# Kernel tuning notes

Measured on AMD Instinct MI355X. Metric: run time of the kernel, lower is better.

## Reference

```python
import jax, jax.numpy as jnp
import numpy as np

BITS = 4
PACK = 32 // BITS  # 8 nibbles per int32
MASK = (1 << BITS) - 1


def _dequant_gptq(qweight, qzeros, scales):
    """GPTQ int4 dequantization matching MixedPrecisionLinear._dequantize_gptq_weight.

    qweight: [OC//PACK, IC] int32 (nibbles packed along output-channel rows)
    qzeros:  [G, IC//PACK]  int32 (nibbles packed along IC columns)
    scales:  [G, IC]        float32
    returns: [OC, IC]       float32 dequantized weight (pre-transpose)
    """
    Rp, IC = qweight.shape
    OC = Rp * PACK
    G = qzeros.shape[0]
    g = OC // G  # group size along OC

    # Unpack weights: row r*PACK + k comes from packed row r, shift k*BITS
    shifts = jnp.arange(PACK, dtype=jnp.int32) * BITS  # [PACK]
    Wq = ((qweight[:, None, :] >> shifts[None, :, None]) & MASK).reshape(OC, IC)

    # Unpack zero points per (group, ic)
    col = jnp.arange(IC, dtype=jnp.int32)
    qz_cols = qzeros[:, col // PACK]                       # [G, IC]
    zp = (qz_cols >> ((col % PACK) * BITS)[None, :]) & MASK  # [G, IC]

    zp_full = jnp.repeat(zp, g, axis=0)                    # [OC, IC]
    scales_full = jnp.repeat(scales, g, axis=0)            # [OC, IC]
    return (Wq - zp_full).astype(jnp.float32) * scales_full


def setup_inputs() -> dict:
    key = jax.random.key(0)
    k0, k1, k2, k3, k4 = jax.random.split(key, 5)
    IN, OUT, G = 4096, 11008, 32   # in_features (OC, packed), out_features (IC), groups
    N = 4096                        # flattened batch*seq tokens
    qweight = jax.random.randint(k0, (IN // PACK, OUT), 0, 2147483647, dtype=jnp.int32)
    qzeros = jax.random.randint(k1, (G, OUT // PACK), 0, 2147483647, dtype=jnp.int32)
    scales = jax.random.uniform(k2, (G, OUT), dtype=jnp.float32) * 0.01
    x = jax.random.normal(k3, (N, IN), dtype=jnp.float32)
    bias = jax.random.normal(k4, (OUT,), dtype=jnp.float32) * 0.01
    return {"input": x, "qweight": qweight, "qzeros": qzeros, "scales": scales, "bias": bias}


def reference(input, qweight, qzeros, scales, bias):
    # W_deq is [OC=in_features, IC=out_features]; the module returns W_deq.t() as the
    # linear weight, so F.linear(input, W_deq.t()) == input @ W_deq + bias.
    W = _dequant_gptq(qweight, qzeros, scales)
    return input @ W + bias
```

## Files before the change

### kernel.cpp

```cpp
#include <hip/hip_runtime.h>
#include <hip/hip_bf16.h>
#include <stdint.h>

#define M_DIM 4096
#define N_DIM 11008
#define K_DIM 4096

typedef float f32x4 __attribute__((ext_vector_type(4)));
typedef __bf16 bf16x8 __attribute__((ext_vector_type(8)));
typedef unsigned short u16x8 __attribute__((ext_vector_type(8)));
typedef unsigned short u16x4 __attribute__((ext_vector_type(4)));

typedef __attribute__((address_space(1))) const unsigned int guint;
typedef __attribute__((address_space(3))) unsigned int luint;
#define GLOAD_LDS16(g, l) \
    __builtin_amdgcn_global_load_lds((guint*)(g), (luint*)(l), 16, 0, 0)

#define WAIT_VM4() asm volatile("s_waitcnt vmcnt(4)" ::: "memory")
#define WAIT_VM0() asm volatile("s_waitcnt vmcnt(0)" ::: "memory")

__device__ __forceinline__ unsigned short f2bf(float f) {
    union { float f; unsigned u; } v; v.f = f;
    return (unsigned short)((v.u + 0x7FFFu + ((v.u >> 16) & 1u)) >> 16);
}

#define DQ_BLOCKS  ((N_DIM / 64) * (K_DIM / 256))
#define CVT_BLOCKS 2048
#define CVT_TOTAL  ((size_t)M_DIM * K_DIM)

__global__ void __launch_bounds__(256) prep_kernel(
    const float* __restrict__ X, const int* __restrict__ QW,
    const int* __restrict__ QZ, const float* __restrict__ SC,
    __hip_bfloat16* __restrict__ Xbf, __hip_bfloat16* __restrict__ Wt)
{
    const int bid = blockIdx.x;
    if (bid >= CVT_BLOCKS) {
        const int db  = bid - CVT_BLOCKS;
        const int bx  = db % (N_DIM / 64);
        const int by  = db / (N_DIM / 64);
        const int n   = bx * 64 + (threadIdx.x & 63);
        const int k64 = by * 4 + (threadIdx.x >> 6);
        const int g   = k64 >> 1;
        const int zp  = ((unsigned)QZ[g * (N_DIM / 8) + (n >> 3)]
                         >> ((n & 7) << 2)) & 15;
        const float sc = SC[g * N_DIM + n];
        const float zs = (float)zp * sc;
        unsigned qv[8];
        #pragma unroll
        for (int r = 0; r < 8; ++r)
            qv[r] = (unsigned)QW[(size_t)(k64 * 8 + r) * N_DIM + n];
        #pragma unroll
        for (int r = 0; r < 8; ++r) {
            bf16x8 h;
            #pragma unroll
            for (int j = 0; j < 8; ++j)
                h[j] = (__bf16)((float)((qv[r] >> (j * 4)) & 15u) * sc - zs);
            *reinterpret_cast<bf16x8*>(Wt + (size_t)n * K_DIM + k64 * 64 + r * 8) = h;
        }
    } else {
        const size_t nthreads = (size_t)CVT_BLOCKS * 256;
        size_t i = ((size_t)bid * 256 + threadIdx.x) * 8;
        const size_t stride = nthreads * 8;
        for (; i < CVT_TOTAL; i += stride) {
            f32x4 a = __builtin_nontemporal_load(
                reinterpret_cast<const f32x4*>(X + i));
            f32x4 b = __builtin_nontemporal_load(
                reinterpret_cast<const f32x4*>(X + i + 4));
            bf16x8 h;
            #pragma unroll
            for (int e = 0; e < 4; ++e) { h[e] = (__bf16)a[e]; h[e + 4] = (__bf16)b[e]; }
            *reinterpret_cast<bf16x8*>(Xbf + i) = h;
        }
    }
}

__global__ void __launch_bounds__(512, 2) gemm_bf16_kernel(
    const __hip_bfloat16* __restrict__ A,
    const __hip_bfloat16* __restrict__ Bt,
    const float* __restrict__ BIAS, float* __restrict__ OUT)
{
    extern __shared__ unsigned char lds[];

    const int tid  = threadIdx.x;
    const int wave = tid >> 6;
    const int lane = tid & 63;
    const int l15  = lane & 15;
    const int lhi  = lane >> 4;
    const int wr   = wave >> 2;
    const int wc   = wave & 3;

    const int bid = blockIdx.x;
    const int swz = (bid & 7) * 86 + (bid >> 3);
    const int m0  = (swz & 15) * 256;
    const int n0  = (swz >> 4) * 256;

    const int pp  = tid >> 3;
    const int so  = (tid & 7) ^ (pp & 7);
    const int grow = pp * 2 + (so >> 2);
    const int klo  = (so & 3) * 8;
    const __hip_bfloat16* Asrc = A  + (size_t)(m0 + grow) * K_DIM + klo;
    const __hip_bfloat16* Bsrc = Bt + (size_t)(n0 + grow) * K_DIM + klo;
    const int t16 = tid * 16;

    const int sws   = (((l15 & 1) << 2) | lhi) ^ ((l15 >> 1) & 7);
    const int lbase = (l15 >> 1) * 128 + sws * 16;
    int aoff[8], boff[4];
    #pragma unroll
    for (int fr = 0; fr < 8; ++fr)
        aoff[fr] = (wr * 128 + fr * 16) * 64 + lbase;
    #pragma unroll
    for (int fc = 0; fc < 4; ++fc)
        boff[fc] = (wc * 64 + fc * 16) * 64 + lbase;

    f32x4 acc[8][4] = {};

    auto stA0 = [&](int c) {
        const int sb = (c & 1) * 65536; const size_t k = (size_t)c * 64;
        GLOAD_LDS16(Asrc + k,                        lds + sb + t16);
        GLOAD_LDS16(Asrc + k + (size_t)128 * K_DIM,  lds + sb + 8192 + t16);
    };
    auto stB0 = [&](int c) {
        const int sb = (c & 1) * 65536; const size_t k = (size_t)c * 64;
        GLOAD_LDS16(Bsrc + k,                        lds + sb + 32768 + t16);
        GLOAD_LDS16(Bsrc + k + (size_t)128 * K_DIM,  lds + sb + 32768 + 8192 + t16);
    };
    auto stA1 = [&](int c) {
        const int sb = (c & 1) * 65536; const size_t k = (size_t)c * 64 + 32;
        GLOAD_LDS16(Asrc + k,                        lds + sb + 16384 + t16);
        GLOAD_LDS16(Asrc + k + (size_t)128 * K_DIM,  lds + sb + 16384 + 8192 + t16);
    };
    auto stB1 = [&](int c) {
        const int sb = (c & 1) * 65536; const size_t k = (size_t)c * 64 + 32;
        GLOAD_LDS16(Bsrc + k,                        lds + sb + 49152 + t16);
        GLOAD_LDS16(Bsrc + k + (size_t)128 * K_DIM,  lds + sb + 49152 + 8192 + t16);
    };

    auto tile = [&](int c, bool st, bool tail) {
        const int buf = (c & 1) * 65536;
        bf16x8 afr[4], bfr[4];
        #pragma unroll
        for (int fc = 0; fc < 4; ++fc)
            bfr[fc] = *reinterpret_cast<const bf16x8*>(lds + buf + 32768 + boff[fc]);
        #pragma unroll
        for (int fr = 0; fr < 4; ++fr)
            afr[fr] = *reinterpret_cast<const bf16x8*>(lds + buf + aoff[fr]);
        if (st) stA0(c + 1);
        __builtin_amdgcn_s_setprio(1);
        #pragma unroll
        for (int fr = 0; fr < 4; ++fr)
            #pragma unroll
            for (int fc = 0; fc < 4; ++fc)
                acc[fr][fc] = __builtin_amdgcn_mfma_f32_16x16x32_bf16(
                    afr[fr], bfr[fc], acc[fr][fc], 0, 0, 0);
        __builtin_amdgcn_s_setprio(0);
        #pragma unroll
        for (int fr = 0; fr < 4; ++fr)
            afr[fr] = *reinterpret_cast<const bf16x8*>(lds + buf + aoff[fr + 4]);
        if (st) stB0(c + 1);
        __builtin_amdgcn_s_setprio(1);
        #pragma unroll
        for (int fr = 0; fr < 4; ++fr)
            #pragma unroll
            for (int fc = 0; fc < 4; ++fc)
                acc[fr + 4][fc] = __builtin_amdgcn_mfma_f32_16x16x32_bf16(
                    afr[fr], bfr[fc], acc[fr + 4][fc], 0, 0, 0);
        __builtin_amdgcn_s_setprio(0);
        if (tail) { WAIT_VM0(); } else { WAIT_VM4(); }
        __builtin_amdgcn_s_barrier();
        #pragma unroll
        for (int fc = 0; fc < 4; ++fc)
            bfr[fc] = *reinterpret_cast<const bf16x8*>(lds + buf + 49152 + boff[fc]);
        #pragma unroll
        for (int fr = 0; fr < 4; ++fr)
            afr[fr] = *reinterpret_cast<const bf16x8*>(lds + buf + 16384 + aoff[fr]);
        if (st) stA1(c + 1);
        __builtin_amdgcn_s_setprio(1);
        #pragma unroll
        for (int fr = 0; fr < 4; ++fr)
            #pragma unroll
            for (int fc = 0; fc < 4; ++fc)
                acc[fr][fc] = __builtin_amdgcn_mfma_f32_16x16x32_bf16(
                    afr[fr], bfr[fc], acc[fr][fc], 0, 0, 0);
        __builtin_amdgcn_s_setprio(0);
        #pragma unroll
        for (int fr = 0; fr < 4; ++fr)
            afr[fr] = *reinterpret_cast<const bf16x8*>(lds + buf + 16384 + aoff[fr + 4]);
        if (st) stB1(c + 1);
        __builtin_amdgcn_s_setprio(1);
        #pragma unroll
        for (int fr = 0; fr < 4; ++fr)
            #pragma unroll
            for (int fc = 0; fc < 4; ++fc)
                acc[fr + 4][fc] = __builtin_amdgcn_mfma_f32_16x16x32_bf16(
                    afr[fr], bfr[fc], acc[fr + 4][fc], 0, 0, 0);
        __builtin_amdgcn_s_setprio(0);
        if (!tail) {
            WAIT_VM4();
            __builtin_amdgcn_s_barrier();
        }
    };

    stA0(0); stB0(0); stA1(0); stB1(0);
    WAIT_VM4();
    __builtin_amdgcn_s_barrier();

    for (int c = 0; c <= 62; ++c)
        tile(c, true, false);
    tile(63, false, true);

    #pragma unroll
    for (int fc = 0; fc < 4; ++fc) {
        const int n    = n0 + wc * 64 + fc * 16 + l15;
        const float bv = BIAS[n];
        #pragma unroll
        for (int fr = 0; fr < 8; ++fr) {
            const int mb = m0 + wr * 128 + fr * 16 + (lhi << 2);
            #pragma unroll
            for (int t = 0; t < 4; ++t)
                __builtin_nontemporal_store(acc[fr][fc][t] + bv,
                    &OUT[(size_t)(mb + t) * N_DIM + n]);
        }
    }
}

__global__ void __launch_bounds__(256) gptq_gemm_kernel(
    const float* __restrict__ X, const int* __restrict__ QW,
    const int* __restrict__ QZ, const float* __restrict__ SC,
    const float* __restrict__ BIAS, float* __restrict__ OUT)
{
    __shared__ __align__(16) unsigned char slds[32768];
    const int tid  = threadIdx.x;
    const int n0   = blockIdx.x * 128;
    const int m0   = blockIdx.y * 128;
    const int wave = tid >> 6;
    const int lane = tid & 63;
    const int wm   = (wave >> 1) * 64;
    const int wn   = (wave & 1) * 64;
    const int l15  = lane & 15;
    const int lhi  = lane >> 4;
    const int arow  = tid >> 4;
    const int acol4 = (tid & 15) << 2;
    const int bnl   = tid & 127;
    const int brb   = tid >> 7;
    const int col   = n0 + bnl;

    f32x4 acc[4][4] = {};
    for (int kt = 0; kt < K_DIM / 64; ++kt) {
        const int k0 = kt * 64;
        #pragma unroll
        for (int r8 = 0; r8 < 8; ++r8) {
            const int row = (r8 << 4) + arow;
            f32x4 v = *reinterpret_cast<const f32x4*>(
                X + (size_t)(m0 + row) * K_DIM + (k0 + acol4));
            u16x4 h;
            #pragma unroll
            for (int e = 0; e < 4; ++e) h[e] = f2bf(v[e]);
            const int bo = row * 128 + ((acol4 << 1) ^ ((row & 7) << 4));
            *reinterpret_cast<u16x4*>(slds + bo) = h;
        }
        {
            const int g    = k0 >> 7;
            const int zp   = (((unsigned)QZ[g * (N_DIM / 8) + (col >> 3)])
                              >> ((col & 7) << 2)) & 15;
            const float sc = SC[g * N_DIM + col];
            const float zs = (float)zp * sc;
            #pragma unroll
            for (int rb = 0; rb < 4; ++rb) {
                const int rl = (rb << 1) + brb;
                const unsigned qw =
                    (unsigned)QW[(size_t)((k0 >> 3) + rl) * N_DIM + col];
                u16x8 h;
                #pragma unroll
                for (int j = 0; j < 8; ++j) {
                    float w = (float)((qw >> (j << 2)) & 15u) * sc - zs;
                    h[j] = f2bf(w);
                }
                const int bo = 16384 + bnl * 128 + ((rl << 4) ^ ((bnl & 7) << 4));
                *reinterpret_cast<u16x8*>(slds + bo) = h;
            }
        }
        __syncthreads();
        #pragma unroll
        for (int kk = 0; kk < 2; ++kk) {
            bf16x8 afr[4], bfr[4];
            #pragma unroll
            for (int i = 0; i < 4; ++i) {
                const int row = wm + (i << 4) + l15;
                afr[i] = *reinterpret_cast<const bf16x8*>(
                    slds + row * 128 + (((kk << 6) + (lhi << 4)) ^ ((row & 7) << 4)));
            }
            #pragma unroll
            for (int j = 0; j < 4; ++j) {
                const int n = wn + (j << 4) + l15;
                bfr[j] = *reinterpret_cast<const bf16x8*>(
                    slds + 16384 + n * 128 + (((kk << 6) + (lhi << 4)) ^ ((n & 7) << 4)));
            }
            #pragma unroll
            for (int i = 0; i < 4; ++i)
                #pragma unroll
                for (int j = 0; j < 4; ++j)
                    acc[i][j] = __builtin_amdgcn_mfma_f32_16x16x32_bf16(
                        afr[i], bfr[j], acc[i][j], 0, 0, 0);
        }
        __syncthreads();
    }
    #pragma unroll
    for (int j = 0; j < 4; ++j) {
        const int n    = n0 + wn + (j << 4) + l15;
        const float bv = BIAS[n];
        #pragma unroll
        for (int i = 0; i < 4; ++i) {
            const int mb = m0 + wm + (i << 4) + (lhi << 2);
            #pragma unroll
            for (int t = 0; t < 4; ++t)
                OUT[(size_t)(mb + t) * N_DIM + n] = acc[i][j][t] + bv;
        }
    }
}

extern "C" void kernel_launch(void* const* d_in, const int* in_sizes, int n_in,
                              void* d_out, int out_size, void* d_ws, size_t ws_size,
                              hipStream_t stream) {
    const float* X  = (const float*)d_in[0];
    const int*   QW = (const int*)d_in[1];
    const int*   QZ = (const int*)d_in[2];
    const float* SC = (const float*)d_in[3];
    const float* BI = (const float*)d_in[4];
    float*      OUT = (float*)d_out;

    const size_t xbf_bytes = (size_t)M_DIM * K_DIM * 2;
    const size_t wt_bytes  = (size_t)N_DIM * K_DIM * 2;

    if (ws_size >= xbf_bytes + wt_bytes) {
        __hip_bfloat16* Xbf = (__hip_bfloat16*)d_ws;
        __hip_bfloat16* Wt  = (__hip_bfloat16*)((char*)d_ws + xbf_bytes);

        prep_kernel<<<DQ_BLOCKS + CVT_BLOCKS, 256, 0, stream>>>(
            X, QW, QZ, SC, Xbf, Wt);
        gemm_bf16_kernel<<<dim3((M_DIM / 256) * (N_DIM / 256)), 512, 131072, stream>>>(
            Xbf, Wt, BI, OUT);
    } else {
        gptq_gemm_kernel<<<dim3(N_DIM / 128, M_DIM / 128), 256, 0, stream>>>(
            X, QW, QZ, SC, BI, OUT);
    }
}
```

Baseline: 378.3 us.

## Shrink GEMM block tile to 256x128 with 4 waves and simpler double buffer

Reworks the bf16 GEMM from 512-thread blocks on 256x256 tiles with a 128KB LDS double buffer into 256-thread blocks on 256x128 tiles with K-step 32 and a 48KB static LDS double buffer. The staging loop is simplified to a prefetch-two-ahead pattern with vmcnt(6) waits and a barrier around each compute step. The aim is more blocks per CU and better latency hiding from lower LDS use. In exchange, each block reuses less data, so global/L2 traffic for A rises, and the extra barriers per K step add synchronisation cost.

After: 471.2 us. 1.25x slower.

```diff
diff --git a/kernel.cpp b/kernel.cpp
--- a/kernel.cpp
+++ b/kernel.cpp
@@ -16,7 +16,7 @@
 #define GLOAD_LDS16(g, l) \
     __builtin_amdgcn_global_load_lds((guint*)(g), (luint*)(l), 16, 0, 0)
 
-#define WAIT_VM4() asm volatile("s_waitcnt vmcnt(4)" ::: "memory")
+#define WAIT_VM6() asm volatile("s_waitcnt vmcnt(6)" ::: "memory")
 #define WAIT_VM0() asm volatile("s_waitcnt vmcnt(0)" ::: "memory")
 
 __device__ __forceinline__ unsigned short f2bf(float f) {
@@ -74,77 +74,63 @@
     }
 }
 
-__global__ void __launch_bounds__(512, 2) gemm_bf16_kernel(
+__global__ void __launch_bounds__(256, 2) gemm_bf16_kernel(
     const __hip_bfloat16* __restrict__ A,
     const __hip_bfloat16* __restrict__ Bt,
     const float* __restrict__ BIAS, float* __restrict__ OUT)
 {
-    extern __shared__ unsigned char lds[];
+    __shared__ __align__(16) unsigned char lds[49152];
 
     const int tid  = threadIdx.x;
     const int wave = tid >> 6;
     const int lane = tid & 63;
     const int l15  = lane & 15;
     const int lhi  = lane >> 4;
-    const int wr   = wave >> 2;
-    const int wc   = wave & 3;
+    const int wr   = wave >> 1;
+    const int wc   = wave & 1;
 
     const int bid = blockIdx.x;
-    const int swz = (bid & 7) * 86 + (bid >> 3);
+    const int swz = (bid & 7) * 172 + (bid >> 3);
     const int m0  = (swz & 15) * 256;
-    const int n0  = (swz >> 4) * 256;
-
-    const int pp  = tid >> 3;
-    const int so  = (tid & 7) ^ (pp & 7);
-    const int grow = pp * 2 + (so >> 2);
-    const int klo  = (so & 3) * 8;
-    const __hip_bfloat16* Asrc = A  + (size_t)(m0 + grow) * K_DIM + klo;
-    const __hip_bfloat16* Bsrc = Bt + (size_t)(n0 + grow) * K_DIM + klo;
-    const int t16 = tid * 16;
-
-    const int sws   = (((l15 & 1) << 2) | lhi) ^ ((l15 >> 1) & 7);
-    const int lbase = (l15 >> 1) * 128 + sws * 16;
+    const int n0  = (swz >> 4) * 128;
+
+    const int arow = tid >> 2;
+    const int kof  = ((tid & 3) ^ ((tid >> 3) & 3)) * 8;
+    const int t16  = tid * 16;
+    const __hip_bfloat16* Asrc = A  + (size_t)(m0 + arow) * K_DIM + kof;
+    const __hip_bfloat16* Bsrc = Bt + (size_t)(n0 + arow) * K_DIM + kof;
+
+    const int sws = (lhi ^ ((l15 >> 1) & 3)) << 4;
     int aoff[8], boff[4];
     #pragma unroll
     for (int fr = 0; fr < 8; ++fr)
-        aoff[fr] = (wr * 128 + fr * 16) * 64 + lbase;
+        aoff[fr] = (wr * 128 + fr * 16 + l15) * 64 + sws;
     #pragma unroll
     for (int fc = 0; fc < 4; ++fc)
-        boff[fc] = (wc * 64 + fc * 16) * 64 + lbase;
+        boff[fc] = 16384 + (wc * 64 + fc * 16 + l15) * 64 + sws;
 
     f32x4 acc[8][4] = {};
 
-    auto stA0 = [&](int c) {
-        const int sb = (c & 1) * 65536; const size_t k = (size_t)c * 64;
-        GLOAD_LDS16(Asrc + k,                        lds + sb + t16);
-        GLOAD_LDS16(Asrc + k + (size_t)128 * K_DIM,  lds + sb + 8192 + t16);
+    auto stage = [&](int c) {
+        const int buf = (c & 1) * 24576;
+        const size_t k = (size_t)c * 32;
+        GLOAD_LDS16(Asrc + k,                        lds + buf + t16);
+        GLOAD_LDS16(Asrc + k + (size_t)64  * K_DIM,  lds + buf + 4096  + t16);
+        GLOAD_LDS16(Asrc + k + (size_t)128 * K_DIM,  lds + buf + 8192  + t16);
+        GLOAD_LDS16(Asrc + k + (size_t)192 * K_DIM,  lds + buf + 12288 + t16);
+        GLOAD_LDS16(Bsrc + k,                        lds + buf + 16384 + t16);
+        GLOAD_LDS16(Bsrc + k + (size_t)64  * K_DIM,  lds + buf + 20480 + t16);
     };
-    auto stB0 = [&](int c) {
-        const int sb = (c & 1) * 65536; const size_t k = (size_t)c * 64;
-        GLOAD_LDS16(Bsrc + k,                        lds + sb + 32768 + t16);
-        GLOAD_LDS16(Bsrc + k + (size_t)128 * K_DIM,  lds + sb + 32768 + 8192 + t16);
-    };
-    auto stA1 = [&](int c) {
-        const int sb = (c & 1) * 65536; const size_t k = (size_t)c * 64 + 32;
-        GLOAD_LDS16(Asrc + k,                        lds + sb + 16384 + t16);
-        GLOAD_LDS16(Asrc + k + (size_t)128 * K_DIM,  lds + sb + 16384 + 8192 + t16);
-    };
-    auto stB1 = [&](int c) {
-        const int sb = (c & 1) * 65536; const size_t k = (size_t)c * 64 + 32;
-        GLOAD_LDS16(Bsrc + k,                        lds + sb + 49152 + t16);
-        GLOAD_LDS16(Bsrc + k + (size_t)128 * K_DIM,  lds + sb + 49152 + 8192 + t16);
-    };
-
-    auto tile = [&](int c, bool st, bool tail) {
-        const int buf = (c & 1) * 65536;
+
+    auto compute = [&](int c) {
+        const int buf = (c & 1) * 24576;
         bf16x8 afr[4], bfr[4];
         #pragma unroll
         for (int fc = 0; fc < 4; ++fc)
-            bfr[fc] = *reinterpret_cast<const bf16x8*>(lds + buf + 32768 + boff[fc]);
+            bfr[fc] = *reinterpret_cast<const bf16x8*>(lds + buf + boff[fc]);
         #pragma unroll
         for (int fr = 0; fr < 4; ++fr)
             afr[fr] = *reinterpret_cast<const bf16x8*>(lds + buf + aoff[fr]);
-        if (st) stA0(c + 1);
         __builtin_amdgcn_s_setprio(1);
         #pragma unroll
         for (int fr = 0; fr < 4; ++fr)
@@ -156,7 +142,6 @@
         #pragma unroll
         for (int fr = 0; fr < 4; ++fr)
             afr[fr] = *reinterpret_cast<const bf16x8*>(lds + buf + aoff[fr + 4]);
-        if (st) stB0(c + 1);
         __builtin_amdgcn_s_setprio(1);
         #pragma unroll
         for (int fr = 0; fr < 4; ++fr)
@@ -165,48 +150,24 @@
                 acc[fr + 4][fc] = __builtin_amdgcn_mfma_f32_16x16x32_bf16(
                     afr[fr], bfr[fc], acc[fr + 4][fc], 0, 0, 0);
         __builtin_amdgcn_s_setprio(0);
-        if (tail) { WAIT_VM0(); } else { WAIT_VM4(); }
+    };
+
+    stage(0); stage(1);
+
+    for (int c = 0; c < 126; ++c) {
+        WAIT_VM6();
         __builtin_amdgcn_s_barrier();
-        #pragma unroll
-        for (int fc = 0; fc < 4; ++fc)
-            bfr[fc] = *reinterpret_cast<const bf16x8*>(lds + buf + 49152 + boff[fc]);
-        #pragma unroll
-        for (int fr = 0; fr < 4; ++fr)
-            afr[fr] = *reinterpret_cast<const bf16x8*>(lds + buf + 16384 + aoff[fr]);
-        if (st) stA1(c + 1);
-        __builtin_amdgcn_s_setprio(1);
-        #pragma unroll
-        for (int fr = 0; fr < 4; ++fr)
-            #pragma unroll
-            for (int fc = 0; fc < 4; ++fc)
-                acc[fr][fc] = __builtin_amdgcn_mfma_f32_16x16x32_bf16(
-                    afr[fr], bfr[fc], acc[fr][fc], 0, 0, 0);
-        __builtin_amdgcn_s_setprio(0);
-        #pragma unroll
-        for (int fr = 0; fr < 4; ++fr)
-            afr[fr] = *reinterpret_cast<const bf16x8*>(lds + buf + 16384 + aoff[fr + 4]);
-        if (st) stB1(c + 1);
-        __builtin_amdgcn_s_setprio(1);
-        #pragma unroll
-        for (int fr = 0; fr < 4; ++fr)
-            #pragma unroll
-            for (int fc = 0; fc < 4; ++fc)
-                acc[fr + 4][fc] = __builtin_amdgcn_mfma_f32_16x16x32_bf16(
-                    afr[fr], bfr[fc], acc[fr + 4][fc], 0, 0, 0);
-        __builtin_amdgcn_s_setprio(0);
-        if (!tail) {
-            WAIT_VM4();
-            __builtin_amdgcn_s_barrier();
-        }
-    };
-
-    stA0(0); stB0(0); stA1(0); stB1(0);
-    WAIT_VM4();
+        compute(c);
+        __builtin_amdgcn_s_barrier();
+        stage(c + 2);
+    }
+    WAIT_VM6();
     __builtin_amdgcn_s_barrier();
-
-    for (int c = 0; c <= 62; ++c)
-        tile(c, true, false);
-    tile(63, false, true);
+    compute(126);
+    __builtin_amdgcn_s_barrier();
+    WAIT_VM0();
+    __builtin_amdgcn_s_barrier();
+    compute(127);
 
     #pragma unroll
     for (int fc = 0; fc < 4; ++fc) {
@@ -337,7 +298,7 @@
 
         prep_kernel<<<DQ_BLOCKS + CVT_BLOCKS, 256, 0, stream>>>(
             X, QW, QZ, SC, Xbf, Wt);
-        gemm_bf16_kernel<<<dim3((M_DIM / 256) * (N_DIM / 256)), 512, 131072, stream>>>(
+        gemm_bf16_kernel<<<dim3((M_DIM / 256) * (N_DIM / 128)), 256, 0, stream>>>(
             Xbf, Wt, BI, OUT);
     } else {
         gptq_gemm_kernel<<<dim3(N_DIM / 128, M_DIM / 128), 256, 0, stream>>>(
```
